# Kernel optimization log

Hardware: AMD Instinct MI355X
Metric: run time of the kernel (lower is better)

Reference implementation:

```python
import jax, jax.numpy as jnp
import numpy as np

L_OUT, B, N, C, M, D, T = 4, 4, 1000, 80, 64, 256, 28
CLS_W, L1_W, GIOU_W, MASK_W = 2.0, 5.0, 2.0, 5.0
ALPHA, GAMMA, EPS = 0.25, 2.0, 1e-8
CANDIDATE_K, CENTER_RADIUS, BIG = 10, 2.5, 100000.0


def _areas(b):
    return (b[..., 2] - b[..., 0]) * (b[..., 3] - b[..., 1])


def pairwise_giou(b1, b2):
    # b1 [n,4], b2 [m,4] -> [n,m] generalized IoU (torchvision convention)
    area1, area2 = _areas(b1), _areas(b2)
    lt = jnp.maximum(b1[:, None, :2], b2[None, :, :2])
    rb = jnp.minimum(b1[:, None, 2:], b2[None, :, 2:])
    wh = jnp.clip(rb - lt, 0.0)
    inter = wh[..., 0] * wh[..., 1]
    union = area1[:, None] + area2[None, :] - inter
    iou = inter / union
    lti = jnp.minimum(b1[:, None, :2], b2[None, :, :2])
    rbi = jnp.maximum(b1[:, None, 2:], b2[None, :, 2:])
    whi = jnp.clip(rbi - lti, 0.0)
    areai = whi[..., 0] * whi[..., 1]
    return iou - (areai - union) / areai


def diag_giou(b1, b2):
    # elementwise giou for matched pairs, b1/b2 [n,4] -> [n]
    area1, area2 = _areas(b1), _areas(b2)
    lt = jnp.maximum(b1[:, :2], b2[:, :2])
    rb = jnp.minimum(b1[:, 2:], b2[:, 2:])
    wh = jnp.clip(rb - lt, 0.0)
    inter = wh[:, 0] * wh[:, 1]
    union = area1 + area2 - inter
    iou = inter / union
    lti = jnp.minimum(b1[:, :2], b2[:, :2])
    rbi = jnp.maximum(b1[:, 2:], b2[:, 2:])
    whi = jnp.clip(rbi - lti, 0.0)
    areai = whi[:, 0] * whi[:, 1]
    return iou - (areai - union) / areai


def pairwise_iou(b1, b2, eps=1e-8):
    # mmdet bbox_overlaps, mode='iou'
    area1, area2 = _areas(b1), _areas(b2)
    lt = jnp.maximum(b1[:, None, :2], b2[None, :, :2])
    rb = jnp.minimum(b1[:, None, 2:], b2[None, :, 2:])
    wh = jnp.clip(rb - lt, 0.0)
    inter = wh[..., 0] * wh[..., 1]
    union = jnp.maximum(area1[:, None] + area2[None, :] - inter, eps)
    return inter / union


def simota_match(logits, boxes, gt_cls, gt_boxes, img_size):
    # SimOTA assignment for one image; fixed shapes via masking instead of boolean indexing
    n, c = logits.shape
    m = gt_boxes.shape[0]
    cx = (boxes[:, 0] + boxes[:, 2]) * 0.5
    cy = (boxes[:, 1] + boxes[:, 3]) * 0.5
    w = boxes[:, 2] - boxes[:, 0]
    h = boxes[:, 3] - boxes[:, 1]
    in_gt = ((cx[:, None] > gt_boxes[None, :, 0]) & (cy[:, None] > gt_boxes[None, :, 1])
             & (cx[:, None] < gt_boxes[None, :, 2]) & (cy[:, None] < gt_boxes[None, :, 3]))
    gcx = (gt_boxes[:, 0] + gt_boxes[:, 2]) * 0.5
    gcy = (gt_boxes[:, 1] + gt_boxes[:, 3]) * 0.5
    rx = CENTER_RADIUS * w[:, None]
    ry = CENTER_RADIUS * h[:, None]
    in_ct = ((cx[:, None] > gcx[None, :] - rx) & (cx[:, None] < gcx[None, :] + rx)
             & (cy[:, None] > gcy[None, :] - ry) & (cy[:, None] < gcy[None, :] + ry))
    valid = in_gt.any(1) | in_ct.any(1)
    in_both = in_gt & in_ct
    has_valid = valid.any()
    valid = valid | (~has_valid)          # fallback: all valid when none
    in_both = in_both | (~has_valid)
    # FocalLossCost (mmdet), weight = cls weight
    p = jax.nn.sigmoid(logits)
    neg = -jnp.log(1.0 - p + EPS) * (1.0 - ALPHA) * p ** GAMMA
    pos = -jnp.log(p + EPS) * ALPHA * (1.0 - p) ** GAMMA
    cls_cost = CLS_W * (pos - neg)[:, gt_cls]          # [n,m]
    nb = boxes / img_size
    ngb = gt_boxes / img_size
    l1_cost = L1_W * jnp.abs(nb[:, None, :] - ngb[None, :, :]).sum(-1)
    giou_cost = GIOU_W * (1.0 - pairwise_giou(nb, ngb))
    cost = cls_cost + l1_cost + giou_cost + (~in_both) * BIG
    cost = jnp.where(valid[:, None], cost, 1e15)       # invalid priors never selected
    ious = pairwise_iou(boxes, gt_boxes) * valid[:, None]
    # dynamic_k_matching
    topk_ious, _ = jax.lax.top_k(ious.T, CANDIDATE_K)  # [m,10]
    dyn_k = jnp.maximum(topk_ious.sum(-1).astype(jnp.int32), 1)
    rank = jnp.argsort(jnp.argsort(cost, axis=0), axis=0)
    matching = rank < dyn_k[None, :]                   # [n,m]
    multi = matching.sum(1) > 1
    best = jnp.argmin(cost, axis=1)
    best_oh = best[:, None] == jnp.arange(m)[None, :]
    matching = jnp.where(multi[:, None], best_oh, matching)
    fg = matching.any(1)
    gt_ind = jnp.argmax(matching, axis=1)
    return fg, gt_ind


def per_image_loss(logits, boxes, pfeat, gt_cls, gt_boxes, gt_masks, img_size, w_mask):
    sg = jax.lax.stop_gradient
    fg, gt_ind = simota_match(sg(logits), sg(boxes), gt_cls, sg(gt_boxes), sg(img_size))
    c = logits.shape[1]
    gcls = gt_cls[gt_ind]
    label = jnp.where(fg[:, None], jax.nn.one_hot(gcls, c, dtype=logits.dtype), 0.0)
    # sigmoid focal loss (sum over all n*c logits)
    p = jax.nn.sigmoid(logits)
    ce = -(label * jax.nn.log_sigmoid(logits) + (1.0 - label) * jax.nn.log_sigmoid(-logits))
    p_t = p * label + (1.0 - p) * (1.0 - label)
    alpha_t = ALPHA * label + (1.0 - ALPHA) * (1.0 - label)
    cls_loss = (alpha_t * ce * (1.0 - p_t) ** GAMMA).sum()
    fgf = fg.astype(logits.dtype)
    nb = boxes / img_size
    gb = gt_boxes[gt_ind] / img_size
    l1_loss = (jnp.abs(nb - gb).sum(-1) * fgf).sum()
    giou_loss = ((1.0 - diag_giou(nb, gb)) * fgf).sum()
    # mask head: per-class mask logits from proposal feats; gather only assigned class
    d = pfeat.shape[1]
    tt = T * T
    w_sel = w_mask.reshape(d, c, tt)[:, gcls, :]        # [d,n,tt]
    m_sel = jax.nn.sigmoid(jnp.einsum('nd,dnt->nt', pfeat, w_sel))
    gm = gt_masks.reshape(gt_masks.shape[0], -1)[gt_ind]  # [n,tt]
    inter = (m_sel * gm).sum(-1)
    union = m_sel.sum(-1) + gm.sum(-1) + 1e-8
    mask_loss = ((1.0 - 2.0 * inter / union) * fgf).sum()
    return cls_loss, l1_loss, giou_loss, mask_loss, fgf.sum()


def _forward(pred_logits, pred_boxes, proposal_feat, gt_boxes, gt_masks, image_size, w_mask, gt_classes):
    per = jax.vmap(per_image_loss, in_axes=(0, 0, 0, 0, 0, 0, 0, None))
    total = jnp.zeros(4, dtype=pred_logits.dtype)
    n_out = pred_logits.shape[0]
    for l in range(n_out):   # small fixed loop over output heads
        cl, l1, gl, ml, k = per(pred_logits[l], pred_boxes[l], proposal_feat[l],
                                gt_classes, gt_boxes, gt_masks, image_size, w_mask)
        num_ins = k.sum()
        total = total + jnp.stack([cl.sum(), l1.sum(), gl.sum(), ml.sum()]) / num_ins
    weights = jnp.array([CLS_W, L1_W, GIOU_W, MASK_W], dtype=total.dtype)
    return weights * total / n_out   # [cls, l1, giou, mask] losses


def setup_inputs():
    key = jax.random.key(0)
    ks = jax.random.split(key, 8)

    def rand_boxes(k, shape):
        k1, k2 = jax.random.split(k)
        ctr = jax.random.uniform(k1, shape + (2,), minval=100.0, maxval=700.0)
        wh = jax.random.uniform(k2, shape + (2,), minval=20.0, maxval=300.0)
        return jnp.concatenate([ctr - wh * 0.5, ctr + wh * 0.5], axis=-1)

    pred_logits = jax.random.normal(ks[0], (L_OUT, B, N, C), dtype=jnp.float32)
    pred_boxes = rand_boxes(ks[1], (L_OUT, B, N))
    proposal_feat = 0.1 * jax.random.normal(ks[2], (L_OUT, B, N, D), dtype=jnp.float32)
    gt_boxes = rand_boxes(ks[3], (B, M))
    gt_masks = (jax.random.uniform(ks[4], (B, M, T, T)) > 0.5).astype(jnp.float32)
    image_size = 800.0 * jnp.ones((B,), dtype=jnp.float32)
    w_mask = 0.02 * jax.random.normal(ks[5], (D, C * T * T), dtype=jnp.float32)
    gt_classes = jax.random.randint(ks[6], (B, M), 0, C)
    return {"pred_logits": pred_logits, "pred_boxes": pred_boxes, "proposal_feat": proposal_feat,
            "gt_boxes": gt_boxes, "gt_masks": gt_masks, "image_size": image_size,
            "w_mask": w_mask, "gt_classes": gt_classes}


def reference(pred_logits, pred_boxes, proposal_feat, gt_boxes, gt_masks, image_size, w_mask, gt_classes):
    return _forward(pred_logits, pred_boxes, proposal_feat, gt_boxes, gt_masks, image_size, w_mask, gt_classes)
```

## Files before the change

kernel.cpp:

```cpp
#include <hip/hip_runtime.h>
#include <math.h>
#include <float.h>

#define LOUT 4
#define BATCH 4
#define NP 1000
#define NC 80
#define NM 64
#define ND 256
#define TT 784
#define NIMG (LOUT*BATCH)
#define CWTT (NC*TT)
#define MAXF (NIMG*NP)
#define CH 16
#define TPT 112
#define MAXCH 768

__device__ __forceinline__ float block_reduce_sum(float v, float* red) {
    int tid = threadIdx.x;
    red[tid] = v; __syncthreads();
    for (int s = blockDim.x >> 1; s > 0; s >>= 1) {
        if (tid < s) red[tid] += red[tid + s];
        __syncthreads();
    }
    float r = red[0]; __syncthreads();
    return r;
}

__global__ void k_valid(const float* __restrict__ boxes, const float* __restrict__ gtb,
                        int* __restrict__ valid, unsigned long long* __restrict__ inboth,
                        int* __restrict__ hasvalid) {
    int img = blockIdx.y;
    int b = img % BATCH;
    int i = blockIdx.x * blockDim.x + threadIdx.x;
    __shared__ float g[NM * 4];
    for (int k = threadIdx.x; k < NM * 4; k += blockDim.x) g[k] = gtb[b * NM * 4 + k];
    __syncthreads();
    if (i >= NP) return;
    float4 bx = *(const float4*)&boxes[((size_t)img * NP + i) * 4];
    float x0 = bx.x, y0 = bx.y, x1 = bx.z, y1 = bx.w;
    float cx = (x0 + x1) * 0.5f, cy = (y0 + y1) * 0.5f;
    float w = x1 - x0, h = y1 - y0;
    float rx = 2.5f * w, ry = 2.5f * h;
    bool any_gt = false, any_ct = false;
    unsigned long long ib = 0ull;
    for (int j = 0; j < NM; ++j) {
        float gx0 = g[j*4], gy0 = g[j*4+1], gx1 = g[j*4+2], gy1 = g[j*4+3];
        bool igt = (cx > gx0) && (cy > gy0) && (cx < gx1) && (cy < gy1);
        float gcx = (gx0 + gx1) * 0.5f, gcy = (gy0 + gy1) * 0.5f;
        bool ict = (cx > gcx - rx) && (cx < gcx + rx) && (cy > gcy - ry) && (cy < gcy + ry);
        any_gt |= igt; any_ct |= ict;
        if (igt && ict) ib |= (1ull << j);
    }
    bool v = any_gt || any_ct;
    valid[img * NP + i] = v ? 1 : 0;
    inboth[img * NP + i] = ib;
    if (v) atomicOr(&hasvalid[img], 1);
}

__global__ void k_cost(const float* __restrict__ logits, const float* __restrict__ boxes,
                       const float* __restrict__ gtb, const int* __restrict__ gcls_all,
                       const float* __restrict__ imsz,
                       const int* __restrict__ valid, const unsigned long long* __restrict__ inboth,
                       const int* __restrict__ hasvalid,
                       float* __restrict__ cost, float* __restrict__ iou_out) {
    int j = blockIdx.x, img = blockIdx.y, b = img % BATCH;
    float s = imsz[b], inv_s = 1.f / s;
    const float* gj = gtb + (b * NM + j) * 4;
    float gx0 = gj[0], gy0 = gj[1], gx1 = gj[2], gy1 = gj[3];
    int gc = gcls_all[b * NM + j];
    int hv = hasvalid[img];
    float garea = (gx1 - gx0) * (gy1 - gy0);
    float ngx0 = gx0 * inv_s, ngy0 = gy0 * inv_s, ngx1 = gx1 * inv_s, ngy1 = gy1 * inv_s;
    float ngarea = (ngx1 - ngx0) * (ngy1 - ngy0);
    size_t colbase = ((size_t)img * NM + j) * NP;
    for (int i = threadIdx.x; i < NP; i += blockDim.x) {
        float4 bx = *(const float4*)&boxes[((size_t)img * NP + i) * 4];
        float x0 = bx.x, y0 = bx.y, x1 = bx.z, y1 = bx.w;
        float area = (x1 - x0) * (y1 - y0);
        float ltx = fmaxf(x0, gx0), lty = fmaxf(y0, gy0);
        float rbx = fminf(x1, gx1), rby = fminf(y1, gy1);
        float iw = fmaxf(rbx - ltx, 0.f), ih = fmaxf(rby - lty, 0.f);
        float inter = iw * ih;
        float uni = fmaxf(area + garea - inter, 1e-8f);
        float iou = inter / uni;
        float nx0 = x0 * inv_s, ny0 = y0 * inv_s, nx1 = x1 * inv_s, ny1 = y1 * inv_s;
        float narea = (nx1 - nx0) * (ny1 - ny0);
        float nltx = fmaxf(nx0, ngx0), nlty = fmaxf(ny0, ngy0);
        float nrbx = fminf(nx1, ngx1), nrby = fminf(ny1, ngy1);
        float niw = fmaxf(nrbx - nltx, 0.f), nih = fmaxf(nrby - nlty, 0.f);
        float ninter = niw * nih;
        float nuni = narea + ngarea - ninter;
        float niou = ninter / nuni;
        float ex0 = fminf(nx0, ngx0), ey0 = fminf(ny0, ngy0);
        float ex1 = fmaxf(nx1, ngx1), ey1 = fmaxf(ny1, ngy1);
        float earea = fmaxf(ex1 - ex0, 0.f) * fmaxf(ey1 - ey0, 0.f);
        float giou = niou - (earea - nuni) / earea;
        float giou_cost = 2.f * (1.f - giou);
        float l1 = 5.f * (fabsf(nx0 - ngx0) + fabsf(ny0 - ngy0) + fabsf(nx1 - ngx1) + fabsf(ny1 - ngy1));
        float x = logits[((size_t)img * NP + i) * NC + gc];
        float p = 1.f / (1.f + expf(-x));
        float neg = -logf(1.f - p + 1e-8f) * 0.75f * p * p;
        float pos = -logf(p + 1e-8f) * 0.25f * (1.f - p) * (1.f - p);
        float cls = 2.f * (pos - neg);
        bool vld = (valid[img * NP + i] != 0) || (hv == 0);
        bool inb = (((inboth[img * NP + i] >> j) & 1ull) != 0ull) || (hv == 0);
        float cst = cls + l1 + giou_cost + (inb ? 0.f : 100000.f);
        if (!vld) cst = 1e15f;
        cost[colbase + i] = cst;
        iou_out[colbase + i] = vld ? iou : 0.f;
    }
}

__global__ void __launch_bounds__(256) k_topk(
        const float* __restrict__ cost, const float* __restrict__ iou,
        float* __restrict__ kthc, int* __restrict__ kthi) {
    int col = blockIdx.x;
    const float* cc = cost + (size_t)col * NP;
    const float* ic = iou + (size_t)col * NP;
    int tid = threadIdx.x;
    float icv[4], ccv[4];
    #pragma unroll
    for (int e = 0; e < 4; ++e) {
        int i = tid + 256 * e;
        bool ok = (i < NP);
        icv[e] = ok ? ic[i] : -FLT_MAX;
        ccv[e] = ok ? cc[i] : FLT_MAX;
    }
    __shared__ float wv[4]; __shared__ int wi[4];
    int wave = tid >> 6, lane = tid & 63;
    unsigned cons = 0;
    float ssum = 0.f;
    for (int it = 0; it < 10; ++it) {
        float bv = -FLT_MAX; int bi = NP;
        #pragma unroll
        for (int e = 0; e < 4; ++e) {
            int i = tid + 256 * e;
            float v = icv[e];
            if (!(cons & (1u << e)) && ((v > bv) || (v == bv && i < bi))) { bv = v; bi = i; }
        }
        #pragma unroll
        for (int s = 1; s < 64; s <<= 1) {
            float ov = __shfl_xor(bv, s, 64);
            int oi = __shfl_xor(bi, s, 64);
            if ((ov > bv) || (ov == bv && oi < bi)) { bv = ov; bi = oi; }
        }
        if (lane == 0) { wv[wave] = bv; wi[wave] = bi; }
        __syncthreads();
        float gv = wv[0]; int gi = wi[0];
        #pragma unroll
        for (int w = 1; w < 4; ++w) {
            float ov = wv[w]; int oi = wi[w];
            if ((ov > gv) || (ov == gv && oi < gi)) { gv = ov; gi = oi; }
        }
        __syncthreads();
        ssum += gv;
        if ((gi & 255) == tid) cons |= (1u << (gi >> 8));
    }
    int dk = (int)ssum; if (dk < 1) dk = 1;
    cons = 0;
    float gvf = 0.f; int gif = 0;
    for (int it = 0; it < dk; ++it) {
        float bv = FLT_MAX; int bi = NP;
        #pragma unroll
        for (int e = 0; e < 4; ++e) {
            int i = tid + 256 * e;
            float v = ccv[e];
            if (!(cons & (1u << e)) && ((v < bv) || (v == bv && i < bi))) { bv = v; bi = i; }
        }
        #pragma unroll
        for (int s = 1; s < 64; s <<= 1) {
            float ov = __shfl_xor(bv, s, 64);
            int oi = __shfl_xor(bi, s, 64);
            if ((ov < bv) || (ov == bv && oi < bi)) { bv = ov; bi = oi; }
        }
        if (lane == 0) { wv[wave] = bv; wi[wave] = bi; }
        __syncthreads();
        float gv = wv[0]; int gi = wi[0];
        #pragma unroll
        for (int w = 1; w < 4; ++w) {
            float ov = wv[w]; int oi = wi[w];
            if ((ov < gv) || (ov == gv && oi < gi)) { gv = ov; gi = oi; }
        }
        __syncthreads();
        if ((gi & 255) == tid) cons |= (1u << (gi >> 8));
        gvf = gv; gif = gi;
    }
    if (tid == 0) { kthc[col] = gvf; kthi[col] = gif; }
}

__global__ void k_match(const float* __restrict__ cost,
                        const float* __restrict__ kthc, const int* __restrict__ kthi,
                        const float* __restrict__ boxes, const float* __restrict__ gtb,
                        const float* __restrict__ imsz, const int* __restrict__ gcls_all,
                        int* __restrict__ fg, int* __restrict__ gt_ind,
                        int* __restrict__ cnt, float* __restrict__ accum) {
    int img = blockIdx.y, b = img % BATCH;
    int i = blockIdx.x * blockDim.x + threadIdx.x;
    __shared__ float skc[NM]; __shared__ int ski[NM];
    __shared__ float red[256];
    if (threadIdx.x < NM) {
        skc[threadIdx.x] = kthc[img * NM + threadIdx.x];
        ski[threadIdx.x] = kthi[img * NM + threadIdx.x];
    }
    __syncthreads();
    float l1 = 0.f, gl = 0.f, f = 0.f;
    if (i < NP) {
        int cntm = 0, first = -1;
        float bc = FLT_MAX; int bj = 0;
        for (int j = 0; j < NM; ++j) {
            float c = cost[((size_t)img * NM + j) * NP + i];
            bool m = (c < skc[j]) || (c == skc[j] && i <= ski[j]);
            if (m) { cntm++; if (first < 0) first = j; }
            if (c < bc) { bc = c; bj = j; }
        }
        int gi = 0, isfg = 0;
        if (cntm > 1) { gi = bj; isfg = 1; }
        else if (cntm == 1) { gi = first; isfg = 1; }
        fg[img * NP + i] = isfg;
        gt_ind[img * NP + i] = gi;
        if (isfg) {
            atomicAdd(&cnt[gcls_all[b * NM + gi]], 1);
            float inv = 1.f / imsz[b];
            float4 bx = *(const float4*)&boxes[((size_t)img * NP + i) * 4];
            const float* gj = gtb + (b * NM + gi) * 4;
            float nx0 = bx.x*inv, ny0 = bx.y*inv, nx1 = bx.z*inv, ny1 = bx.w*inv;
            float gx0 = gj[0]*inv, gy0 = gj[1]*inv, gx1 = gj[2]*inv, gy1 = gj[3]*inv;
            l1 = fabsf(nx0-gx0) + fabsf(ny0-gy0) + fabsf(nx1-gx1) + fabsf(ny1-gy1);
            float a1 = (nx1-nx0)*(ny1-ny0), a2 = (gx1-gx0)*(gy1-gy0);
            float ltx = fmaxf(nx0,gx0), lty = fmaxf(ny0,gy0);
            float rbx = fminf(nx1,gx1), rby = fminf(ny1,gy1);
            float iw = fmaxf(rbx-ltx,0.f), ih = fmaxf(rby-lty,0.f);
            float inter = iw*ih, uni = a1+a2-inter, iou = inter/uni;
            float ex0 = fminf(nx0,gx0), ey0 = fminf(ny0,gy0);
            float ex1 = fmaxf(nx1,gx1), ey1 = fmaxf(ny1,gy1);
            float ea = fmaxf(ex1-ex0,0.f)*fmaxf(ey1-ey0,0.f);
            float giou = iou - (ea-uni)/ea;
            gl = 1.f - giou;
            f = 1.f;
        }
    }
    float sl1 = block_reduce_sum(l1, red);
    float sgl = block_reduce_sum(gl, red);
    float sf  = block_reduce_sum(f, red);
    if (threadIdx.x == 0) {
        atomicAdd(&accum[img*5+1], sl1);
        atomicAdd(&accum[img*5+2], sgl);
        atomicAdd(&accum[img*5+4], sf);
    }
}

__global__ void k_focal(const float* __restrict__ logits, const int* __restrict__ fg,
                        const int* __restrict__ gt_ind, const int* __restrict__ gcls_all,
                        float* __restrict__ accum) {
    int img = blockIdx.y, b = img % BATCH;
    int idx = blockIdx.x * blockDim.x + threadIdx.x;
    __shared__ float red[256];
    float v = 0.f;
    if (idx < NP * NC) {
        int i = idx / NC, c = idx % NC;
        float x = logits[(size_t)img * NP * NC + idx];
        int lab = 0;
        if (fg[img * NP + i]) {
            int gc = gcls_all[b * NM + gt_ind[img * NP + i]];
            lab = (c == gc) ? 1 : 0;
        }
        float p = 1.f / (1.f + expf(-x));
        float ax = fabsf(x);
        float sp = log1pf(expf(-ax));
        float ls_pos = fminf(x, 0.f) - sp;
        float ls_neg = fminf(-x, 0.f) - sp;
        if (lab) v = 0.25f * (-ls_pos) * (1.f - p) * (1.f - p);
        else     v = 0.75f * (-ls_neg) * p * p;
    }
    float sv = block_reduce_sum(v, red);
    if (threadIdx.x == 0) atomicAdd(&accum[img*5+0], sv);
}

__global__ void k_gmsum(const float* __restrict__ gtm, float* __restrict__ gmsum) {
    int bj = blockIdx.x;
    __shared__ float red[128];
    float s = 0.f;
    for (int t = threadIdx.x; t < TT; t += 128) s += gtm[(size_t)bj * TT + t];
    int tid = threadIdx.x;
    red[tid] = s; __syncthreads();
    for (int st = 64; st > 0; st >>= 1) {
        if (tid < st) red[tid] += red[tid + st];
        __syncthreads();
    }
    if (tid == 0) gmsum[bj] = red[0];
}

__global__ void k_scan(const int* __restrict__ cnt, int* __restrict__ offs,
                       int* __restrict__ total, int* __restrict__ chtab, int* __restrict__ nch) {
    if (threadIdx.x == 0 && blockIdx.x == 0) {
        int s = 0;
        for (int c = 0; c < NC; ++c) { offs[c] = s; s += cnt[c]; }
        *total = s;
        int m = 0;
        for (int c = 0; c < NC; ++c) {
            int nchc = (cnt[c] + CH - 1) / CH;
            for (int k = 0; k < nchc; ++k) chtab[m++] = (c << 16) | k;
        }
        *nch = m;
    }
}

__global__ void k_scatter(const int* __restrict__ fg, const int* __restrict__ gti,
                          const int* __restrict__ gcls, const int* __restrict__ offs,
                          int* __restrict__ fill, int* __restrict__ list) {
    int idx = blockIdx.x * 256 + threadIdx.x;
    if (idx >= NIMG * NP) return;
    int img = idx / NP, i = idx % NP, b = img % BATCH;
    if (fg[idx]) {
        int gt = gti[idx];
        int c = gcls[b * NM + gt];
        int pos = offs[c] + atomicAdd(&fill[c], 1);
        list[pos] = (img << 16) | (gt << 10) | i;
    }
}

__global__ void __launch_bounds__(128) k_mgemm(
        const float* __restrict__ pfeat, const float* __restrict__ wmask,
        const float* __restrict__ gtm, const int* __restrict__ list,
        const int* __restrict__ cnt, const int* __restrict__ offs,
        const int* __restrict__ chtab, const int* __restrict__ nch,
        float* __restrict__ inter, float* __restrict__ msum) {
    int ch = blockIdx.x;
    if (ch >= *nch) return;
    int e = chtab[ch];
    int c = e >> 16, k = e & 0xffff;
    int base = offs[c] + k * CH;
    int P = min(CH, cnt[c] - k * CH);
    int tid = threadIdx.x;
    bool act = (tid < TPT);
    int t = blockIdx.y * TPT + (act ? tid : 0);
    __shared__ float pf[CH][ND];
    __shared__ int sl[CH];
    if (tid < CH) sl[tid] = (tid < P) ? list[base + tid] : 0;
    __syncthreads();
    for (int idx = tid; idx < CH * (ND / 4); idx += 128) {
        int p = idx >> 6, d4 = idx & 63;
        float4 v = {0.f, 0.f, 0.f, 0.f};
        if (p < P) {
            int pk = sl[p];
            int img = pk >> 16, i = pk & 1023;
            v = *(const float4*)&pfeat[((size_t)img * NP + i) * ND + d4 * 4];
        }
        *(float4*)&pf[p][d4 * 4] = v;
    }
    __syncthreads();
    float acc[CH];
    #pragma unroll
    for (int p = 0; p < CH; ++p) acc[p] = 0.f;
    if (act) {
        const float* wr = wmask + (size_t)c * TT + t;
        float4 wq[4];
        #pragma unroll
        for (int q = 0; q < 4; ++q) {
            const float* wp = wr + (size_t)q * 4 * CWTT;
            wq[q].x = wp[0]; wq[q].y = wp[CWTT];
            wq[q].z = wp[2 * (size_t)CWTT]; wq[q].w = wp[3 * (size_t)CWTT];
        }
        #pragma unroll 4
        for (int d4 = 0; d4 < 60; ++d4) {
            float4 w = wq[d4 & 3];
            const float* wp = wr + (size_t)(d4 + 4) * 4 * CWTT;
            wq[d4 & 3].x = wp[0]; wq[d4 & 3].y = wp[CWTT];
            wq[d4 & 3].z = wp[2 * (size_t)CWTT]; wq[d4 & 3].w = wp[3 * (size_t)CWTT];
            int d = d4 * 4;
            #pragma unroll
            for (int p = 0; p < CH; ++p) {
                float4 q4 = *(const float4*)&pf[p][d];
                acc[p] += q4.x * w.x + q4.y * w.y + q4.z * w.z + q4.w * w.w;
            }
        }
        #pragma unroll
        for (int d4 = 60; d4 < 64; ++d4) {
            float4 w = wq[d4 & 3];
            int d = d4 * 4;
            #pragma unroll
            for (int p = 0; p < CH; ++p) {
                float4 q4 = *(const float4*)&pf[p][d];
                acc[p] += q4.x * w.x + q4.y * w.y + q4.z * w.z + q4.w * w.w;
            }
        }
    }
    #pragma unroll 4
    for (int p = 0; p < CH; ++p) {
        if (p >= P) break;
        int pk = sl[p];
        int img = pk >> 16, j = (pk >> 10) & 63, b = img % BATCH;
        float li = 0.f, lm = 0.f;
        if (act) {
            float m = 1.f / (1.f + expf(-acc[p]));
            float g = gtm[((size_t)(b * NM + j)) * TT + t];
            li = m * g; lm = m;
        }
        #pragma unroll
        for (int s = 32; s > 0; s >>= 1) {
            li += __shfl_down(li, s, 64);
            lm += __shfl_down(lm, s, 64);
        }
        if ((tid & 63) == 0) {
            atomicAdd(&inter[base + p], li);
            atomicAdd(&msum[base + p], lm);
        }
    }
}

__global__ void __launch_bounds__(256) k_dicefinal(
        const int* __restrict__ list, const int* __restrict__ total,
        const float* __restrict__ inter, const float* __restrict__ msum,
        const float* __restrict__ gmsum, const float* __restrict__ accum,
        float* __restrict__ out) {
    __shared__ float md[NIMG];
    int tid = threadIdx.x;
    if (tid < NIMG) md[tid] = 0.f;
    __syncthreads();
    int n = *total;
    for (int e = tid; e < n; e += 256) {
        int pk = list[e];
        int img = pk >> 16, j = (pk >> 10) & 63, b = img % BATCH;
        float d = 1.f - 2.f * inter[e] / (msum[e] + gmsum[b * NM + j] + 1e-8f);
        atomicAdd(&md[img], d);
    }
    __syncthreads();
    if (tid == 0) {
        float tot[4] = {0.f, 0.f, 0.f, 0.f};
        for (int l = 0; l < LOUT; ++l) {
            float s0 = 0.f, s1 = 0.f, s2 = 0.f, s3 = 0.f, s4 = 0.f;
            for (int b = 0; b < BATCH; ++b) {
                int img = l * BATCH + b;
                s0 += accum[img*5+0]; s1 += accum[img*5+1]; s2 += accum[img*5+2];
                s3 += md[img];        s4 += accum[img*5+4];
            }
            tot[0] += s0 / s4; tot[1] += s1 / s4; tot[2] += s2 / s4; tot[3] += s3 / s4;
        }
        const float w[4] = {2.f, 5.f, 2.f, 5.f};
        for (int k = 0; k < 4; ++k) out[k] = w[k] * tot[k] / (float)LOUT;
    }
}

extern "C" void kernel_launch(void* const* d_in, const int* in_sizes, int n_in,
                              void* d_out, int out_size, void* d_ws, size_t ws_size,
                              hipStream_t stream) {
    const float* logits = (const float*)d_in[0];
    const float* boxes  = (const float*)d_in[1];
    const float* pfeat  = (const float*)d_in[2];
    const float* gtb    = (const float*)d_in[3];
    const float* gtm    = (const float*)d_in[4];
    const float* imsz   = (const float*)d_in[5];
    const float* wmask  = (const float*)d_in[6];
    const int*   gcls   = (const int*)d_in[7];

    char* ws = (char*)d_ws;
    size_t off = 0;
    auto alloc = [&](size_t bytes) -> void* {
        void* p = ws + off;
        off = (off + bytes + 255) & ~(size_t)255;
        return p;
    };
    char* zbase = ws;
    float* accum = (float*)alloc(NIMG * 5 * sizeof(float));
    int* cnt    = (int*)alloc(NC * sizeof(int));
    int* fill   = (int*)alloc(NC * sizeof(int));
    int* hasvalid = (int*)alloc(NIMG * sizeof(int));
    float* interA = (float*)alloc((size_t)MAXF * sizeof(float));
    float* msumA  = (float*)alloc((size_t)MAXF * sizeof(float));
    size_t zbytes = off;
    float* cost = (float*)alloc((size_t)NIMG * NM * NP * sizeof(float));
    float* iou  = (float*)alloc((size_t)NIMG * NM * NP * sizeof(float));
    int* valid  = (int*)alloc((size_t)NIMG * NP * sizeof(int));
    unsigned long long* inboth = (unsigned long long*)alloc((size_t)NIMG * NP * sizeof(unsigned long long));
    float* kthc = (float*)alloc(NIMG * NM * sizeof(float));
    int* kthi   = (int*)alloc(NIMG * NM * sizeof(int));
    int* fg     = (int*)alloc((size_t)NIMG * NP * sizeof(int));
    int* gti    = (int*)alloc((size_t)NIMG * NP * sizeof(int));
    float* gmsum = (float*)alloc(BATCH * NM * sizeof(float));
    int* offs   = (int*)alloc(NC * sizeof(int));
    int* total  = (int*)alloc(sizeof(int));
    int* nch    = (int*)alloc(sizeof(int));
    int* chtab  = (int*)alloc((size_t)MAXCH * sizeof(int));
    int* list   = (int*)alloc((size_t)MAXF * sizeof(int));

    hipMemsetAsync(zbase, 0, zbytes, stream);

    k_valid<<<dim3((NP + 255) / 256, NIMG), 256, 0, stream>>>(boxes, gtb, valid, inboth, hasvalid);
    k_cost<<<dim3(NM, NIMG), 256, 0, stream>>>(logits, boxes, gtb, gcls, imsz, valid, inboth, hasvalid, cost, iou);
    k_topk<<<NIMG * NM, 256, 0, stream>>>(cost, iou, kthc, kthi);
    k_match<<<dim3((NP + 255) / 256, NIMG), 256, 0, stream>>>(cost, kthc, kthi, boxes, gtb, imsz, gcls, fg, gti, cnt, accum);
    k_focal<<<dim3((NP * NC + 255) / 256, NIMG), 256, 0, stream>>>(logits, fg, gti, gcls, accum);
    k_gmsum<<<BATCH * NM, 128, 0, stream>>>(gtm, gmsum);
    k_scan<<<1, 64, 0, stream>>>(cnt, offs, total, chtab, nch);
    k_scatter<<<(NIMG * NP + 255) / 256, 256, 0, stream>>>(fg, gti, gcls, offs, fill, list);
    k_mgemm<<<dim3(MAXCH, (TT + TPT - 1) / TPT), 128, 0, stream>>>(pfeat, wmask, gtm, list, cnt, offs, chtab, nch, interA, msumA);
    k_dicefinal<<<1, 256, 0, stream>>>(list, total, interA, msumA, gmsum, accum, (float*)d_out);
}
```

Baseline: 221.3 us.

## Fuse cost with top-k, merge scan with scatter, and double mask-GEMM chunk size

The cost computation now feeds the dynamic-k top-k selection directly from registers in one kernel, so the IoU matrix is no longer written to and re-read from global memory. The scan and scatter kernels are merged into one single-block kernel that uses shared-memory fill counters, which removes a launch and the global fill buffer. The mask GEMM chunk size is doubled with a matching lower chunk-table bound, and gmsum is launched first. Risks: the single 1024-thread scatter block serialises a pass over all images, and larger chunks can leave more padded work in partially filled chunks.

```diff
diff --git a/kernel.cpp b/kernel.cpp
--- a/kernel.cpp
+++ b/kernel.cpp
@@ -12,9 +12,9 @@
 #define NIMG (LOUT*BATCH)
 #define CWTT (NC*TT)
 #define MAXF (NIMG*NP)
-#define CH 16
+#define CH 32
 #define TPT 112
-#define MAXCH 768
+#define MAXCH 408
 
 __device__ __forceinline__ float block_reduce_sum(float v, float* red) {
     int tid = threadIdx.x;
@@ -58,12 +58,13 @@
     if (v) atomicOr(&hasvalid[img], 1);
 }
 
-__global__ void k_cost(const float* __restrict__ logits, const float* __restrict__ boxes,
-                       const float* __restrict__ gtb, const int* __restrict__ gcls_all,
-                       const float* __restrict__ imsz,
-                       const int* __restrict__ valid, const unsigned long long* __restrict__ inboth,
-                       const int* __restrict__ hasvalid,
-                       float* __restrict__ cost, float* __restrict__ iou_out) {
+__global__ void __launch_bounds__(256) k_costtopk(
+        const float* __restrict__ logits, const float* __restrict__ boxes,
+        const float* __restrict__ gtb, const int* __restrict__ gcls_all,
+        const float* __restrict__ imsz,
+        const int* __restrict__ valid, const unsigned long long* __restrict__ inboth,
+        const int* __restrict__ hasvalid,
+        float* __restrict__ cost, float* __restrict__ kthc, int* __restrict__ kthi) {
     int j = blockIdx.x, img = blockIdx.y, b = img % BATCH;
     float s = imsz[b], inv_s = 1.f / s;
     const float* gj = gtb + (b * NM + j) * 4;
@@ -74,58 +75,51 @@
     float ngx0 = gx0 * inv_s, ngy0 = gy0 * inv_s, ngx1 = gx1 * inv_s, ngy1 = gy1 * inv_s;
     float ngarea = (ngx1 - ngx0) * (ngy1 - ngy0);
     size_t colbase = ((size_t)img * NM + j) * NP;
-    for (int i = threadIdx.x; i < NP; i += blockDim.x) {
-        float4 bx = *(const float4*)&boxes[((size_t)img * NP + i) * 4];
-        float x0 = bx.x, y0 = bx.y, x1 = bx.z, y1 = bx.w;
-        float area = (x1 - x0) * (y1 - y0);
-        float ltx = fmaxf(x0, gx0), lty = fmaxf(y0, gy0);
-        float rbx = fminf(x1, gx1), rby = fminf(y1, gy1);
-        float iw = fmaxf(rbx - ltx, 0.f), ih = fmaxf(rby - lty, 0.f);
-        float inter = iw * ih;
-        float uni = fmaxf(area + garea - inter, 1e-8f);
-        float iou = inter / uni;
-        float nx0 = x0 * inv_s, ny0 = y0 * inv_s, nx1 = x1 * inv_s, ny1 = y1 * inv_s;
-        float narea = (nx1 - nx0) * (ny1 - ny0);
-        float nltx = fmaxf(nx0, ngx0), nlty = fmaxf(ny0, ngy0);
-        float nrbx = fminf(nx1, ngx1), nrby = fminf(ny1, ngy1);
-        float niw = fmaxf(nrbx - nltx, 0.f), nih = fmaxf(nrby - nlty, 0.f);
-        float ninter = niw * nih;
-        float nuni = narea + ngarea - ninter;
-        float niou = ninter / nuni;
-        float ex0 = fminf(nx0, ngx0), ey0 = fminf(ny0, ngy0);
-        float ex1 = fmaxf(nx1, ngx1), ey1 = fmaxf(ny1, ngy1);
-        float earea = fmaxf(ex1 - ex0, 0.f) * fmaxf(ey1 - ey0, 0.f);
-        float giou = niou - (earea - nuni) / earea;
-        float giou_cost = 2.f * (1.f - giou);
-        float l1 = 5.f * (fabsf(nx0 - ngx0) + fabsf(ny0 - ngy0) + fabsf(nx1 - ngx1) + fabsf(ny1 - ngy1));
-        float x = logits[((size_t)img * NP + i) * NC + gc];
-        float p = 1.f / (1.f + expf(-x));
-        float neg = -logf(1.f - p + 1e-8f) * 0.75f * p * p;
-        float pos = -logf(p + 1e-8f) * 0.25f * (1.f - p) * (1.f - p);
-        float cls = 2.f * (pos - neg);
-        bool vld = (valid[img * NP + i] != 0) || (hv == 0);
-        bool inb = (((inboth[img * NP + i] >> j) & 1ull) != 0ull) || (hv == 0);
-        float cst = cls + l1 + giou_cost + (inb ? 0.f : 100000.f);
-        if (!vld) cst = 1e15f;
-        cost[colbase + i] = cst;
-        iou_out[colbase + i] = vld ? iou : 0.f;
-    }
-}
-
-__global__ void __launch_bounds__(256) k_topk(
-        const float* __restrict__ cost, const float* __restrict__ iou,
-        float* __restrict__ kthc, int* __restrict__ kthi) {
-    int col = blockIdx.x;
-    const float* cc = cost + (size_t)col * NP;
-    const float* ic = iou + (size_t)col * NP;
     int tid = threadIdx.x;
     float icv[4], ccv[4];
     #pragma unroll
     for (int e = 0; e < 4; ++e) {
         int i = tid + 256 * e;
-        bool ok = (i < NP);
-        icv[e] = ok ? ic[i] : -FLT_MAX;
-        ccv[e] = ok ? cc[i] : FLT_MAX;
+        if (i < NP) {
+            float4 bx = *(const float4*)&boxes[((size_t)img * NP + i) * 4];
+            float x0 = bx.x, y0 = bx.y, x1 = bx.z, y1 = bx.w;
+            float area = (x1 - x0) * (y1 - y0);
+            float ltx = fmaxf(x0, gx0), lty = fmaxf(y0, gy0);
+            float rbx = fminf(x1, gx1), rby = fminf(y1, gy1);
+            float iw = fmaxf(rbx - ltx, 0.f), ih = fmaxf(rby - lty, 0.f);
+            float inter = iw * ih;
+            float uni = fmaxf(area + garea - inter, 1e-8f);
+            float iou = inter / uni;
+            float nx0 = x0 * inv_s, ny0 = y0 * inv_s, nx1 = x1 * inv_s, ny1 = y1 * inv_s;
+            float narea = (nx1 - nx0) * (ny1 - ny0);
+            float nltx = fmaxf(nx0, ngx0), nlty = fmaxf(ny0, ngy0);
+            float nrbx = fminf(nx1, ngx1), nrby = fminf(ny1, ngy1);
+            float niw = fmaxf(nrbx - nltx, 0.f), nih = fmaxf(nrby - nlty, 0.f);
+            float ninter = niw * nih;
+            float nuni = narea + ngarea - ninter;
+            float niou = ninter / nuni;
+            float ex0 = fminf(nx0, ngx0), ey0 = fminf(ny0, ngy0);
+            float ex1 = fmaxf(nx1, ngx1), ey1 = fmaxf(ny1, ngy1);
+            float earea = fmaxf(ex1 - ex0, 0.f) * fmaxf(ey1 - ey0, 0.f);
+            float giou = niou - (earea - nuni) / earea;
+            float giou_cost = 2.f * (1.f - giou);
+            float l1 = 5.f * (fabsf(nx0 - ngx0) + fabsf(ny0 - ngy0) + fabsf(nx1 - ngx1) + fabsf(ny1 - ngy1));
+            float x = logits[((size_t)img * NP + i) * NC + gc];
+            float p = 1.f / (1.f + expf(-x));
+            float neg = -logf(1.f - p + 1e-8f) * 0.75f * p * p;
+            float pos = -logf(p + 1e-8f) * 0.25f * (1.f - p) * (1.f - p);
+            float cls = 2.f * (pos - neg);
+            bool vld = (valid[img * NP + i] != 0) || (hv == 0);
+            bool inb = (((inboth[img * NP + i] >> j) & 1ull) != 0ull) || (hv == 0);
+            float cst = cls + l1 + giou_cost + (inb ? 0.f : 100000.f);
+            if (!vld) cst = 1e15f;
+            cost[colbase + i] = cst;
+            ccv[e] = cst;
+            icv[e] = vld ? iou : 0.f;
+        } else {
+            ccv[e] = FLT_MAX;
+            icv[e] = -FLT_MAX;
+        }
     }
     __shared__ float wv[4]; __shared__ int wi[4];
     int wave = tid >> 6, lane = tid & 63;
@@ -140,9 +134,9 @@
             if (!(cons & (1u << e)) && ((v > bv) || (v == bv && i < bi))) { bv = v; bi = i; }
         }
         #pragma unroll
-        for (int s = 1; s < 64; s <<= 1) {
-            float ov = __shfl_xor(bv, s, 64);
-            int oi = __shfl_xor(bi, s, 64);
+        for (int sft = 1; sft < 64; sft <<= 1) {
+            float ov = __shfl_xor(bv, sft, 64);
+            int oi = __shfl_xor(bi, sft, 64);
             if ((ov > bv) || (ov == bv && oi < bi)) { bv = ov; bi = oi; }
         }
         if (lane == 0) { wv[wave] = bv; wi[wave] = bi; }
@@ -169,9 +163,9 @@
             if (!(cons & (1u << e)) && ((v < bv) || (v == bv && i < bi))) { bv = v; bi = i; }
         }
         #pragma unroll
-        for (int s = 1; s < 64; s <<= 1) {
-            float ov = __shfl_xor(bv, s, 64);
-            int oi = __shfl_xor(bi, s, 64);
+        for (int sft = 1; sft < 64; sft <<= 1) {
+            float ov = __shfl_xor(bv, sft, 64);
+            int oi = __shfl_xor(bi, sft, 64);
             if ((ov < bv) || (ov == bv && oi < bi)) { bv = ov; bi = oi; }
         }
         if (lane == 0) { wv[wave] = bv; wi[wave] = bi; }
@@ -186,7 +180,7 @@
         if ((gi & 255) == tid) cons |= (1u << (gi >> 8));
         gvf = gv; gif = gi;
     }
-    if (tid == 0) { kthc[col] = gvf; kthi[col] = gif; }
+    if (tid == 0) { kthc[blockIdx.y * NM + j] = gvf; kthi[blockIdx.y * NM + j] = gif; }
 }
 
 __global__ void k_match(const float* __restrict__ cost,
@@ -291,32 +285,36 @@
     if (tid == 0) gmsum[bj] = red[0];
 }
 
-__global__ void k_scan(const int* __restrict__ cnt, int* __restrict__ offs,
-                       int* __restrict__ total, int* __restrict__ chtab, int* __restrict__ nch) {
-    if (threadIdx.x == 0 && blockIdx.x == 0) {
-        int s = 0;
-        for (int c = 0; c < NC; ++c) { offs[c] = s; s += cnt[c]; }
-        *total = s;
-        int m = 0;
+__global__ void __launch_bounds__(1024) k_scanscatter(
+        const int* __restrict__ cnt, const int* __restrict__ fg,
+        const int* __restrict__ gti, const int* __restrict__ gcls,
+        int* __restrict__ offs_g, int* __restrict__ total,
+        int* __restrict__ chtab, int* __restrict__ nch, int* __restrict__ list) {
+    __shared__ int offs[NC]; __shared__ int choff[NC]; __shared__ int sfill[NC];
+    int tid = threadIdx.x;
+    if (tid == 0) {
+        int s = 0, m = 0;
         for (int c = 0; c < NC; ++c) {
-            int nchc = (cnt[c] + CH - 1) / CH;
-            for (int k = 0; k < nchc; ++k) chtab[m++] = (c << 16) | k;
-        }
-        *nch = m;
-    }
-}
-
-__global__ void k_scatter(const int* __restrict__ fg, const int* __restrict__ gti,
-                          const int* __restrict__ gcls, const int* __restrict__ offs,
-                          int* __restrict__ fill, int* __restrict__ list) {
-    int idx = blockIdx.x * 256 + threadIdx.x;
-    if (idx >= NIMG * NP) return;
-    int img = idx / NP, i = idx % NP, b = img % BATCH;
-    if (fg[idx]) {
-        int gt = gti[idx];
-        int c = gcls[b * NM + gt];
-        int pos = offs[c] + atomicAdd(&fill[c], 1);
-        list[pos] = (img << 16) | (gt << 10) | i;
+            offs[c] = s; s += cnt[c];
+            choff[c] = m; m += (cnt[c] + CH - 1) / CH;
+        }
+        *total = s; *nch = m;
+    }
+    if (tid < NC) sfill[tid] = 0;
+    __syncthreads();
+    if (tid < NC) {
+        offs_g[tid] = offs[tid];
+        int n = cnt[tid], co = choff[tid];
+        for (int k = 0; k * CH < n; ++k) chtab[co + k] = (tid << 16) | k;
+    }
+    for (int idx = tid; idx < NIMG * NP; idx += 1024) {
+        if (fg[idx]) {
+            int img = idx / NP, i = idx % NP, b = img % BATCH;
+            int gt = gti[idx];
+            int c = gcls[b * NM + gt];
+            int pos = offs[c] + atomicAdd(&sfill[c], 1);
+            list[pos] = (img << 16) | (gt << 10) | i;
+        }
     }
 }
 
@@ -464,13 +462,11 @@
     char* zbase = ws;
     float* accum = (float*)alloc(NIMG * 5 * sizeof(float));
     int* cnt    = (int*)alloc(NC * sizeof(int));
-    int* fill   = (int*)alloc(NC * sizeof(int));
     int* hasvalid = (int*)alloc(NIMG * sizeof(int));
     float* interA = (float*)alloc((size_t)MAXF * sizeof(float));
     float* msumA  = (float*)alloc((size_t)MAXF * sizeof(float));
     size_t zbytes = off;
     float* cost = (float*)alloc((size_t)NIMG * NM * NP * sizeof(float));
-    float* iou  = (float*)alloc((size_t)NIMG * NM * NP * sizeof(float));
     int* valid  = (int*)alloc((size_t)NIMG * NP * sizeof(int));
     unsigned long long* inboth = (unsigned long long*)alloc((size_t)NIMG * NP * sizeof(unsigned long long));
     float* kthc = (float*)alloc(NIMG * NM * sizeof(float));
@@ -486,14 +482,12 @@
 
     hipMemsetAsync(zbase, 0, zbytes, stream);
 
+    k_gmsum<<<BATCH * NM, 128, 0, stream>>>(gtm, gmsum);
     k_valid<<<dim3((NP + 255) / 256, NIMG), 256, 0, stream>>>(boxes, gtb, valid, inboth, hasvalid);
-    k_cost<<<dim3(NM, NIMG), 256, 0, stream>>>(logits, boxes, gtb, gcls, imsz, valid, inboth, hasvalid, cost, iou);
-    k_topk<<<NIMG * NM, 256, 0, stream>>>(cost, iou, kthc, kthi);
+    k_costtopk<<<dim3(NM, NIMG), 256, 0, stream>>>(logits, boxes, gtb, gcls, imsz, valid, inboth, hasvalid, cost, kthc, kthi);
     k_match<<<dim3((NP + 255) / 256, NIMG), 256, 0, stream>>>(cost, kthc, kthi, boxes, gtb, imsz, gcls, fg, gti, cnt, accum);
     k_focal<<<dim3((NP * NC + 255) / 256, NIMG), 256, 0, stream>>>(logits, fg, gti, gcls, accum);
-    k_gmsum<<<BATCH * NM, 128, 0, stream>>>(gtm, gmsum);
-    k_scan<<<1, 64, 0, stream>>>(cnt, offs, total, chtab, nch);
-    k_scatter<<<(NIMG * NP + 255) / 256, 256, 0, stream>>>(fg, gti, gcls, offs, fill, list);
+    k_scanscatter<<<1, 1024, 0, stream>>>(cnt, fg, gti, gcls, offs, total, chtab, nch, list);
     k_mgemm<<<dim3(MAXCH, (TT + TPT - 1) / TPT), 128, 0, stream>>>(pfeat, wmask, gtm, list, cnt, offs, chtab, nch, interA, msumA);
     k_dicefinal<<<1, 256, 0, stream>>>(list, total, interA, msumA, gmsum, accum, (float*)d_out);
 }
```

After: 237.4 us. 1.07x slower.
